# Kernel tuning notes

Measured on AMD Instinct MI355X. Metric: run time of the kernel, lower is better.

The kernel has to match this reference:

```python
import jax, jax.numpy as jnp
import numpy as np

N = 50000
E = 800000
D = 64  # d_s


def _mlp2(x, w1, b1, w2, b2):
    # Linear -> SiLU -> Linear
    return jax.nn.silu(x @ w1 + b1) @ w2 + b2


def setup_inputs() -> dict:
    key = jax.random.key(0)
    ks = jax.random.split(key, 20)
    s = jax.random.normal(ks[0], (N, D), jnp.float32)
    v = jax.random.normal(ks[1], (N, 3), jnp.float32)
    edge_index = jax.random.randint(ks[2], (2, E), 0, N, jnp.int32)
    edge_attr = jax.random.normal(ks[3], (E, D), jnp.float32)
    ev = jax.random.normal(ks[4], (E, 3), jnp.float32)
    edge_vec_unit = ev / jnp.linalg.norm(ev, axis=-1, keepdims=True)

    def lin(k, fan_in, fan_out):
        kw, kb = jax.random.split(k)
        lim = 1.0 / np.sqrt(fan_in)
        w = jax.random.uniform(kw, (fan_in, fan_out), jnp.float32, -lim, lim)
        b = jax.random.uniform(kb, (fan_out,), jnp.float32, -lim, lim)
        return w, b

    ng_w1, ng_b1 = lin(ks[5], D + 1, D)
    ng_w2, ng_b2 = lin(ks[6], D, D)
    eg_w1, eg_b1 = lin(ks[7], D + 1, D)
    eg_w2, eg_b2 = lin(ks[8], D, D)
    mg_w1, mg_b1 = lin(ks[9], 3 * D, 2 * D)
    mg_w2, mg_b2 = lin(ks[10], 2 * D, D)
    pe_w, pe_b = lin(ks[11], D, 1)
    up_w, up_b = lin(ks[12], D, D)
    ln_g = jnp.ones((D,), jnp.float32)
    ln_b = jnp.zeros((D,), jnp.float32)
    return dict(s=s, v=v, edge_index=edge_index, edge_attr=edge_attr,
                edge_vec_unit=edge_vec_unit,
                ng_w1=ng_w1, ng_b1=ng_b1, ng_w2=ng_w2, ng_b2=ng_b2,
                eg_w1=eg_w1, eg_b1=eg_b1, eg_w2=eg_w2, eg_b2=eg_b2,
                mg_w1=mg_w1, mg_b1=mg_b1, mg_w2=mg_w2, mg_b2=mg_b2,
                pe_w=pe_w, pe_b=pe_b, up_w=up_w, up_b=up_b,
                ln_g=ln_g, ln_b=ln_b)


def reference(s, v, edge_index, edge_attr, edge_vec_unit,
              ng_w1, ng_b1, ng_w2, ng_b2,
              eg_w1, eg_b1, eg_w2, eg_b2,
              mg_w1, mg_b1, mg_w2, mg_b2,
              pe_w, pe_b, up_w, up_b, ln_g, ln_b):
    row, col = edge_index[0], edge_index[1]
    s_i, s_j = s[row], s[col]            # (E, D)
    v_i, v_j = v[row], v[col]            # (E, 3)

    dot_ij = jnp.sum(v_i * edge_vec_unit, axis=-1, keepdims=True)
    dot_ji = jnp.sum(v_j * -edge_vec_unit, axis=-1, keepdims=True)
    res_ij = 1.0 - dot_ij
    res_ji = 1.0 - dot_ji
    cross_mag = jnp.linalg.norm(jnp.cross(v_i, v_j), axis=-1, keepdims=True)

    node_feat_i = _mlp2(jnp.concatenate([s_i, res_ij], -1), ng_w1, ng_b1, ng_w2, ng_b2)
    node_feat_j = _mlp2(jnp.concatenate([s_j, res_ji], -1), ng_w1, ng_b1, ng_w2, ng_b2)
    edge_feat = _mlp2(jnp.concatenate([edge_attr, cross_mag], -1), eg_w1, eg_b1, eg_w2, eg_b2)

    msg = _mlp2(jnp.concatenate([node_feat_i, node_feat_j, edge_feat], -1),
                mg_w1, mg_b1, mg_w2, mg_b2)   # (E, D)
    coeff = msg @ pe_w + pe_b                 # (E, 1)
    v_msg = edge_vec_unit * coeff             # (E, 3)

    n = s.shape[0]
    s_agg = jax.ops.segment_sum(msg, row, num_segments=n)    # (N, D)
    v_agg = jax.ops.segment_sum(v_msg, row, num_segments=n)  # (N, 3)

    s_new = s + jax.nn.silu(s_agg) @ up_w + up_b
    mu = jnp.mean(s_new, axis=-1, keepdims=True)
    var = jnp.var(s_new, axis=-1, keepdims=True)
    s_out = (s_new - mu) * jax.lax.rsqrt(var + 1e-5) * ln_g + ln_b

    v_new = v + v_agg
    denom = jnp.maximum(jnp.linalg.norm(v_new, axis=-1, keepdims=True), 1e-6)
    v_out = v_new / denom
    return (s_out, v_out)
```

## Files before the change

### kernel.cpp

```cpp
#include <hip/hip_runtime.h>
#include <math.h>

#define NN 50000
#define NE 800000
#define D 64

typedef __attribute__((ext_vector_type(8))) short short8;
typedef __attribute__((ext_vector_type(4))) float f32x4;

__device__ __forceinline__ float silu_f(float x) { return x / (1.0f + __expf(-x)); }

__device__ __forceinline__ unsigned int pack2(float a, float b) {
  unsigned int r;
  asm("v_cvt_pk_bf16_f32 %0, %1, %2" : "=v"(r) : "v"(a), "v"(b));
  return r;
}
__device__ __forceinline__ short8 pack_frag(f32x4 a, f32x4 b) {
  union { unsigned int u[4]; short8 s; } r;
  r.u[0] = pack2(a[0], a[1]);
  r.u[1] = pack2(a[2], a[3]);
  r.u[2] = pack2(b[0], b[1]);
  r.u[3] = pack2(b[2], b[3]);
  return r.s;
}

__global__ void prep_all(const float* __restrict__ ng_w2,
                         const float* __restrict__ eg_w1,
                         const float* __restrict__ eg_w2,
                         const float* __restrict__ mg_w1,
                         const float* __restrict__ mg_w2,
                         const float* __restrict__ ng_w1,
                         const float* __restrict__ up_w,
                         unsigned short* __restrict__ out) {
  int t = blockIdx.x * 256 + threadIdx.x;
  if (t >= 104 * 64) return;
  int frag = t >> 6, L = t & 63;
  const float* W; int K, N, f0;
  if (frag < 8)       { W = ng_w2; K = 64;  N = 64;  f0 = 0; }
  else if (frag < 16) { W = eg_w1; K = 64;  N = 64;  f0 = 8; }
  else if (frag < 24) { W = eg_w2; K = 64;  N = 64;  f0 = 16; }
  else if (frag < 72) { W = mg_w1; K = 192; N = 128; f0 = 24; }
  else if (frag < 88) { W = mg_w2; K = 128; N = 64;  f0 = 72; }
  else if (frag < 96) { W = ng_w1; K = 64;  N = 64;  f0 = 88; }
  else                { W = up_w;  K = 64;  N = 64;  f0 = 96; }
  int lf = frag - f0;
  int kd = K >> 5;
  int nt = lf / kd, ks = lf % kd;
  int kb = ks * 32 + (L >> 4) * 8;
  int nc = nt * 16 + (L & 15);
  unsigned int p[4];
#pragma unroll
  for (int jj = 0; jj < 4; ++jj) {
    float a = W[(size_t)(kb + 2 * jj) * N + nc];
    float b = W[(size_t)(kb + 2 * jj + 1) * N + nc];
    p[jj] = pack2(a, b);
  }
  *(uint4*)(out + (size_t)frag * 512 + L * 8) = make_uint4(p[0], p[1], p[2], p[3]);
}

__global__ __launch_bounds__(256, 4) void node_pre(
    const float* __restrict__ s, const float* __restrict__ ng_b1,
    const unsigned short* __restrict__ WF, float* __restrict__ h_ng,
    float* __restrict__ s_agg, float* __restrict__ v_agg) {
  __shared__ __align__(16) char sm[4 * 8704];
  int tid = threadIdx.x, w = tid >> 6, lane = tid & 63;
  int l15 = lane & 15, q = lane >> 4, fb = q * 8;
  char* my = sm + w * 8704;
  int nb = (blockIdx.x * 4 + w) * 32;
  if (nb >= NN) return;

  short8 Bs[2][2];
#pragma unroll
  for (int h = 0; h < 2; ++h)
#pragma unroll
    for (int kt = 0; kt < 2; ++kt) {
      int n = nb + h * 16 + l15; if (n >= NN) n = NN - 1;
      f32x4 x0 = *(const f32x4*)(s + (size_t)n * D + kt * 32 + fb);
      f32x4 x1 = *(const f32x4*)(s + (size_t)n * D + kt * 32 + fb + 4);
      Bs[h][kt] = pack_frag(x0, x1);
    }
  short8 F[4][2]; f32x4 bb[4];
#pragma unroll
  for (int mt = 0; mt < 4; ++mt) {
    F[mt][0] = *(const short8*)(WF + (size_t)(88 + mt * 2 + 0) * 512 + lane * 8);
    F[mt][1] = *(const short8*)(WF + (size_t)(88 + mt * 2 + 1) * 512 + lane * 8);
    bb[mt] = *(const f32x4*)(ng_b1 + mt * 16 + 4 * q);
  }
#pragma unroll
  for (int h = 0; h < 2; ++h)
#pragma unroll
    for (int mt = 0; mt < 4; ++mt) {
      f32x4 acc = {0.f, 0.f, 0.f, 0.f};
      acc = __builtin_amdgcn_mfma_f32_16x16x32_bf16(F[mt][0], Bs[h][0], acc, 0, 0, 0);
      acc = __builtin_amdgcn_mfma_f32_16x16x32_bf16(F[mt][1], Bs[h][1], acc, 0, 0, 0);
      acc[0] += bb[mt][0]; acc[1] += bb[mt][1]; acc[2] += bb[mt][2]; acc[3] += bb[mt][3];
      *(f32x4*)(my + (((h * 16 + l15) * 68 + mt * 16 + 4 * q) << 2)) = acc;
    }
#pragma unroll
  for (int h = 0; h < 2; ++h)
#pragma unroll
    for (int e = 0; e < 16; ++e) {
      int n = nb + h * 16 + e;
      if (n < NN) {
        float val = *(const float*)(my + (((h * 16 + e) * 68 + lane) << 2));
        h_ng[(size_t)n * D + lane] = val;
        s_agg[(size_t)n * D + lane] = 0.f;
      }
    }
#pragma unroll
  for (int h = 0; h < 2; ++h) {
    int n = nb + h * 16 + l15;
    if (q < 3 && n < NN) v_agg[(size_t)n * 3 + q] = 0.f;
  }
}

#define LSTR 100
#define LDSW (32 * LSTR * 4)

__global__ __launch_bounds__(256, 3) void edge_mfma(
    const float* __restrict__ v, const int* __restrict__ ei,
    const float* __restrict__ edge_attr, const float* __restrict__ evu,
    const float* __restrict__ ng_w1, const float* __restrict__ ng_b2,
    const float* __restrict__ eg_w1, const float* __restrict__ eg_b1,
    const float* __restrict__ eg_b2,
    const float* __restrict__ mg_b1, const float* __restrict__ mg_b2,
    const float* __restrict__ pe_w, const float* __restrict__ pe_b,
    const float* __restrict__ h_ng,
    const unsigned short* __restrict__ WF,
    float* __restrict__ s_agg, float* __restrict__ v_agg) {
  __shared__ __align__(16) char sm[4 * LDSW];
  int tid = threadIdx.x, w = tid >> 6, lane = tid & 63;
  int l15 = lane & 15, q = lane >> 4, fb = q * 8;
  char* my = sm + w * LDSW;
  int eb = (blockIdx.x * 4 + w) * 32;

  int rown[2], coln[2];
  float rij[2], rji[2], uu0[2], uu1[2], uu2[2], cmag[2];
#pragma unroll
  for (int h = 0; h < 2; ++h) {
    int e = eb + h * 16 + l15;
    int r = ei[e], c = ei[NE + e];
    rown[h] = r; coln[h] = c;
    float u0 = evu[e * 3 + 0], u1 = evu[e * 3 + 1], u2 = evu[e * 3 + 2];
    uu0[h] = u0; uu1[h] = u1; uu2[h] = u2;
    float vi0 = v[r * 3 + 0], vi1 = v[r * 3 + 1], vi2 = v[r * 3 + 2];
    float vj0 = v[c * 3 + 0], vj1 = v[c * 3 + 1], vj2 = v[c * 3 + 2];
    rij[h] = 1.f - (vi0 * u0 + vi1 * u1 + vi2 * u2);
    rji[h] = 1.f + (vj0 * u0 + vj1 * u1 + vj2 * u2);
    float cx = vi1 * vj2 - vi2 * vj1;
    float cy = vi2 * vj0 - vi0 * vj2;
    float cz = vi0 * vj1 - vi1 * vj0;
    cmag[h] = sqrtf(cx * cx + cy * cy + cz * cz);
  }

  short8 Bai[2][2], Baj[2][2], Bxe[2][2];
  f32x4 w1l[2][2];
#pragma unroll
  for (int kt = 0; kt < 2; ++kt) {
    w1l[kt][0] = *(const f32x4*)(ng_w1 + 64 * 64 + kt * 32 + fb);
    w1l[kt][1] = *(const f32x4*)(ng_w1 + 64 * 64 + kt * 32 + fb + 4);
  }
#pragma unroll
  for (int h = 0; h < 2; ++h)
#pragma unroll
    for (int kt = 0; kt < 2; ++kt) {
      const float* pr = h_ng + (size_t)rown[h] * D + kt * 32 + fb;
      const float* pc = h_ng + (size_t)coln[h] * D + kt * 32 + fb;
      const float* px = edge_attr + (size_t)(eb + h * 16 + l15) * D + kt * 32 + fb;
      f32x4 a0 = *(const f32x4*)pr, a1 = *(const f32x4*)(pr + 4);
      f32x4 b0 = *(const f32x4*)pc, b1 = *(const f32x4*)(pc + 4);
      f32x4 x0 = *(const f32x4*)px, x1 = *(const f32x4*)(px + 4);
      f32x4 si0, si1, sj0, sj1;
#pragma unroll
      for (int c2 = 0; c2 < 4; ++c2) {
        si0[c2] = silu_f(a0[c2] + rij[h] * w1l[kt][0][c2]);
        si1[c2] = silu_f(a1[c2] + rij[h] * w1l[kt][1][c2]);
        sj0[c2] = silu_f(b0[c2] + rji[h] * w1l[kt][0][c2]);
        sj1[c2] = silu_f(b1[c2] + rji[h] * w1l[kt][1][c2]);
      }
      Bai[h][kt] = pack_frag(si0, si1);
      Baj[h][kt] = pack_frag(sj0, sj1);
      Bxe[h][kt] = pack_frag(x0, x1);
    }

  {
    short8 F[4][2]; f32x4 bb[4];
#pragma unroll
    for (int mt = 0; mt < 4; ++mt) {
      F[mt][0] = *(const short8*)(WF + (size_t)(0 + mt * 2 + 0) * 512 + lane * 8);
      F[mt][1] = *(const short8*)(WF + (size_t)(0 + mt * 2 + 1) * 512 + lane * 8);
      bb[mt] = *(const f32x4*)(ng_b2 + mt * 16 + 4 * q);
    }
#pragma unroll
    for (int h = 0; h < 2; ++h)
#pragma unroll
      for (int mt = 0; mt < 4; ++mt) {
        f32x4 ai = {0.f, 0.f, 0.f, 0.f}, aj = {0.f, 0.f, 0.f, 0.f};
        ai = __builtin_amdgcn_mfma_f32_16x16x32_bf16(F[mt][0], Bai[h][0], ai, 0, 0, 0);
        ai = __builtin_amdgcn_mfma_f32_16x16x32_bf16(F[mt][1], Bai[h][1], ai, 0, 0, 0);
        aj = __builtin_amdgcn_mfma_f32_16x16x32_bf16(F[mt][0], Baj[h][0], aj, 0, 0, 0);
        aj = __builtin_amdgcn_mfma_f32_16x16x32_bf16(F[mt][1], Baj[h][1], aj, 0, 0, 0);
        uint2 pi, pj;
        pi.x = pack2(ai[0] + bb[mt][0], ai[1] + bb[mt][1]);
        pi.y = pack2(ai[2] + bb[mt][2], ai[3] + bb[mt][3]);
        pj.x = pack2(aj[0] + bb[mt][0], aj[1] + bb[mt][1]);
        pj.y = pack2(aj[2] + bb[mt][2], aj[3] + bb[mt][3]);
        int row = h * 16 + l15;
        *(uint2*)(my + ((row * LSTR + mt * 8 + 2 * q) << 2)) = pi;
        *(uint2*)(my + ((row * LSTR + 32 + mt * 8 + 2 * q) << 2)) = pj;
      }
  }

  {
    short8 F[4][2]; f32x4 bb[4], el[4];
#pragma unroll
    for (int mt = 0; mt < 4; ++mt) {
      F[mt][0] = *(const short8*)(WF + (size_t)(8 + mt * 2 + 0) * 512 + lane * 8);
      F[mt][1] = *(const short8*)(WF + (size_t)(8 + mt * 2 + 1) * 512 + lane * 8);
      bb[mt] = *(const f32x4*)(eg_b1 + mt * 16 + 4 * q);
      el[mt] = *(const f32x4*)(eg_w1 + 64 * 64 + mt * 16 + 4 * q);
    }
#pragma unroll
    for (int h = 0; h < 2; ++h)
#pragma unroll
      for (int mt = 0; mt < 4; ++mt) {
        f32x4 acc = {0.f, 0.f, 0.f, 0.f};
        acc = __builtin_amdgcn_mfma_f32_16x16x32_bf16(F[mt][0], Bxe[h][0], acc, 0, 0, 0);
        acc = __builtin_amdgcn_mfma_f32_16x16x32_bf16(F[mt][1], Bxe[h][1], acc, 0, 0, 0);
        float t0 = silu_f(acc[0] + bb[mt][0] + cmag[h] * el[mt][0]);
        float t1 = silu_f(acc[1] + bb[mt][1] + cmag[h] * el[mt][1]);
        float t2 = silu_f(acc[2] + bb[mt][2] + cmag[h] * el[mt][2]);
        float t3 = silu_f(acc[3] + bb[mt][3] + cmag[h] * el[mt][3]);
        uint2 p; p.x = pack2(t0, t1); p.y = pack2(t2, t3);
        *(uint2*)(my + (((h * 16 + l15) * LSTR + 64 + mt * 8 + 2 * q) << 2)) = p;
      }
  }

  {
    short8 Bae[2][2];
#pragma unroll
    for (int h = 0; h < 2; ++h)
#pragma unroll
      for (int kt = 0; kt < 2; ++kt)
        Bae[h][kt] = *(const short8*)(my + (((h * 16 + l15) * LSTR + 64 + 16 * kt + 4 * q) << 2));
    short8 F[4][2]; f32x4 bb[4];
#pragma unroll
    for (int mt = 0; mt < 4; ++mt) {
      F[mt][0] = *(const short8*)(WF + (size_t)(16 + mt * 2 + 0) * 512 + lane * 8);
      F[mt][1] = *(const short8*)(WF + (size_t)(16 + mt * 2 + 1) * 512 + lane * 8);
      bb[mt] = *(const f32x4*)(eg_b2 + mt * 16 + 4 * q);
    }
#pragma unroll
    for (int h = 0; h < 2; ++h)
#pragma unroll
      for (int mt = 0; mt < 4; ++mt) {
        f32x4 acc = {0.f, 0.f, 0.f, 0.f};
        acc = __builtin_amdgcn_mfma_f32_16x16x32_bf16(F[mt][0], Bae[h][0], acc, 0, 0, 0);
        acc = __builtin_amdgcn_mfma_f32_16x16x32_bf16(F[mt][1], Bae[h][1], acc, 0, 0, 0);
        uint2 p;
        p.x = pack2(acc[0] + bb[mt][0], acc[1] + bb[mt][1]);
        p.y = pack2(acc[2] + bb[mt][2], acc[3] + bb[mt][3]);
        *(uint2*)(my + (((h * 16 + l15) * LSTR + 64 + mt * 8 + 2 * q) << 2)) = p;
      }
  }

  {
    short8 Bin[2][6];
#pragma unroll
    for (int h = 0; h < 2; ++h)
#pragma unroll
      for (int kt = 0; kt < 6; ++kt)
        Bin[h][kt] = *(const short8*)(my + (((h * 16 + l15) * LSTR + 16 * kt + 4 * q) << 2));
#pragma unroll
    for (int mt = 0; mt < 8; ++mt) {
      short8 F[6];
#pragma unroll
      for (int ks = 0; ks < 6; ++ks)
        F[ks] = *(const short8*)(WF + (size_t)(24 + mt * 6 + ks) * 512 + lane * 8);
      f32x4 bb = *(const f32x4*)(mg_b1 + mt * 16 + 4 * q);
#pragma unroll
      for (int h = 0; h < 2; ++h) {
        f32x4 acc = {0.f, 0.f, 0.f, 0.f};
#pragma unroll
        for (int ks = 0; ks < 6; ++ks)
          acc = __builtin_amdgcn_mfma_f32_16x16x32_bf16(F[ks], Bin[h][ks], acc, 0, 0, 0);
        uint2 p;
        p.x = pack2(silu_f(acc[0] + bb[0]), silu_f(acc[1] + bb[1]));
        p.y = pack2(silu_f(acc[2] + bb[2]), silu_f(acc[3] + bb[3]));
        *(uint2*)(my + (((h * 16 + l15) * LSTR + mt * 8 + 2 * q) << 2)) = p;
      }
    }
  }

  f32x4 msg[2][4];
  {
    short8 Bh[2][4];
#pragma unroll
    for (int h = 0; h < 2; ++h)
#pragma unroll
      for (int kt = 0; kt < 4; ++kt)
        Bh[h][kt] = *(const short8*)(my + (((h * 16 + l15) * LSTR + 16 * kt + 4 * q) << 2));
#pragma unroll
    for (int mt = 0; mt < 4; ++mt) {
      short8 F[4];
#pragma unroll
      for (int ks = 0; ks < 4; ++ks)
        F[ks] = *(const short8*)(WF + (size_t)(72 + mt * 4 + ks) * 512 + lane * 8);
      f32x4 bb = *(const f32x4*)(mg_b2 + mt * 16 + 4 * q);
#pragma unroll
      for (int h = 0; h < 2; ++h) {
        f32x4 acc = {0.f, 0.f, 0.f, 0.f};
#pragma unroll
        for (int ks = 0; ks < 4; ++ks)
          acc = __builtin_amdgcn_mfma_f32_16x16x32_bf16(F[ks], Bh[h][ks], acc, 0, 0, 0);
        acc[0] += bb[0]; acc[1] += bb[1]; acc[2] += bb[2]; acc[3] += bb[3];
        msg[h][mt] = acc;
      }
    }
  }

  float part[2] = {0.f, 0.f};
#pragma unroll
  for (int mt = 0; mt < 4; ++mt) {
    f32x4 pw4 = *(const f32x4*)(pe_w + mt * 16 + 4 * q);
#pragma unroll
    for (int h = 0; h < 2; ++h)
      part[h] += msg[h][mt][0] * pw4[0] + msg[h][mt][1] * pw4[1] +
                 msg[h][mt][2] * pw4[2] + msg[h][mt][3] * pw4[3];
  }
  float peb = pe_b[0];
#pragma unroll
  for (int h = 0; h < 2; ++h) {
    part[h] += __shfl_xor(part[h], 16, 64);
    part[h] += __shfl_xor(part[h], 32, 64);
    if (q < 3) {
      float uc = (q == 0) ? uu0[h] : ((q == 1) ? uu1[h] : uu2[h]);
      atomicAdd(&v_agg[(size_t)rown[h] * 3 + q], uc * (part[h] + peb));
    }
  }

#pragma unroll
  for (int h = 0; h < 2; ++h)
#pragma unroll
    for (int mt = 0; mt < 4; ++mt)
      *(f32x4*)(my + (((h * 16 + l15) * LSTR + mt * 16 + 4 * q) << 2)) = msg[h][mt];
#pragma unroll
  for (int h = 0; h < 2; ++h)
#pragma unroll
    for (int e = 0; e < 16; ++e) {
      int sr = __builtin_amdgcn_readlane(rown[h], e);
      float val = *(const float*)(my + (((h * 16 + e) * LSTR + lane) << 2));
      atomicAdd(&s_agg[(size_t)sr * D + lane], val);
    }
}

__global__ __launch_bounds__(256, 4) void node_out(
    const float* __restrict__ s, const float* __restrict__ v,
    const float* __restrict__ up_b,
    const float* __restrict__ ln_g, const float* __restrict__ ln_b,
    const float* __restrict__ s_agg, const float* __restrict__ v_agg,
    const unsigned short* __restrict__ WF, float* __restrict__ out) {
  __shared__ __align__(16) char sm[4 * 8704];
  int tid = threadIdx.x, w = tid >> 6, lane = tid & 63;
  int l15 = lane & 15, q = lane >> 4, fb = q * 8;
  char* my = sm + w * 8704;
  int nb = (blockIdx.x * 4 + w) * 32;
  if (nb >= NN) return;

  short8 Bg[2][2];
#pragma unroll
  for (int h = 0; h < 2; ++h)
#pragma unroll
    for (int kt = 0; kt < 2; ++kt) {
      int n = nb + h * 16 + l15; if (n >= NN) n = NN - 1;
      f32x4 g0 = *(const f32x4*)(s_agg + (size_t)n * D + kt * 32 + fb);
      f32x4 g1 = *(const f32x4*)(s_agg + (size_t)n * D + kt * 32 + fb + 4);
#pragma unroll
      for (int c2 = 0; c2 < 4; ++c2) { g0[c2] = silu_f(g0[c2]); g1[c2] = silu_f(g1[c2]); }
      Bg[h][kt] = pack_frag(g0, g1);
    }
  short8 F[4][2]; f32x4 bb[4];
#pragma unroll
  for (int mt = 0; mt < 4; ++mt) {
    F[mt][0] = *(const short8*)(WF + (size_t)(96 + mt * 2 + 0) * 512 + lane * 8);
    F[mt][1] = *(const short8*)(WF + (size_t)(96 + mt * 2 + 1) * 512 + lane * 8);
    bb[mt] = *(const f32x4*)(up_b + mt * 16 + 4 * q);
  }
  f32x4 sn[2][4];
#pragma unroll
  for (int h = 0; h < 2; ++h) {
    int n = nb + h * 16 + l15; if (n >= NN) n = NN - 1;
#pragma unroll
    for (int mt = 0; mt < 4; ++mt) {
      f32x4 acc = {0.f, 0.f, 0.f, 0.f};
      acc = __builtin_amdgcn_mfma_f32_16x16x32_bf16(F[mt][0], Bg[h][0], acc, 0, 0, 0);
      acc = __builtin_amdgcn_mfma_f32_16x16x32_bf16(F[mt][1], Bg[h][1], acc, 0, 0, 0);
      f32x4 sv = *(const f32x4*)(s + (size_t)n * D + mt * 16 + 4 * q);
      sn[h][mt][0] = acc[0] + bb[mt][0] + sv[0];
      sn[h][mt][1] = acc[1] + bb[mt][1] + sv[1];
      sn[h][mt][2] = acc[2] + bb[mt][2] + sv[2];
      sn[h][mt][3] = acc[3] + bb[mt][3] + sv[3];
    }
  }
#pragma unroll
  for (int h = 0; h < 2; ++h) {
    float m = 0.f;
#pragma unroll
    for (int mt = 0; mt < 4; ++mt)
      m += sn[h][mt][0] + sn[h][mt][1] + sn[h][mt][2] + sn[h][mt][3];
    m += __shfl_xor(m, 16, 64);
    m += __shfl_xor(m, 32, 64);
    float mu = m * (1.f / 64.f);
    float vv = 0.f;
#pragma unroll
    for (int mt = 0; mt < 4; ++mt)
#pragma unroll
      for (int r = 0; r < 4; ++r) {
        float d = sn[h][mt][r] - mu;
        vv += d * d;
      }
    vv += __shfl_xor(vv, 16, 64);
    vv += __shfl_xor(vv, 32, 64);
    float inv = 1.f / sqrtf(vv * (1.f / 64.f) + 1e-5f);
#pragma unroll
    for (int mt = 0; mt < 4; ++mt) {
      f32x4 lg = *(const f32x4*)(ln_g + mt * 16 + 4 * q);
      f32x4 lb = *(const f32x4*)(ln_b + mt * 16 + 4 * q);
      f32x4 ov;
#pragma unroll
      for (int r = 0; r < 4; ++r) ov[r] = (sn[h][mt][r] - mu) * inv * lg[r] + lb[r];
      *(f32x4*)(my + (((h * 16 + l15) * 68 + mt * 16 + 4 * q) << 2)) = ov;
    }
  }
#pragma unroll
  for (int h = 0; h < 2; ++h)
#pragma unroll
    for (int e = 0; e < 16; ++e) {
      int n = nb + h * 16 + e;
      if (n < NN) {
        float val = *(const float*)(my + (((h * 16 + e) * 68 + lane) << 2));
        out[(size_t)n * D + lane] = val;
      }
    }
#pragma unroll
  for (int h = 0; h < 2; ++h) {
    int n = nb + h * 16 + l15;
    if (q < 3 && n < NN) {
      float v0 = v[n * 3 + 0] + v_agg[(size_t)n * 3 + 0];
      float v1 = v[n * 3 + 1] + v_agg[(size_t)n * 3 + 1];
      float v2 = v[n * 3 + 2] + v_agg[(size_t)n * 3 + 2];
      float nrm = sqrtf(v0 * v0 + v1 * v1 + v2 * v2);
      float denom = fmaxf(nrm, 1e-6f);
      float val = (q == 0) ? v0 : ((q == 1) ? v1 : v2);
      out[(size_t)NN * D + (size_t)n * 3 + q] = val / denom;
    }
  }
}

extern "C" void kernel_launch(void* const* d_in, const int* in_sizes, int n_in,
                              void* d_out, int out_size, void* d_ws, size_t ws_size,
                              hipStream_t stream) {
  const float* s         = (const float*)d_in[0];
  const float* v         = (const float*)d_in[1];
  const int*   ei        = (const int*)d_in[2];
  const float* edge_attr = (const float*)d_in[3];
  const float* evu       = (const float*)d_in[4];
  const float* ng_w1     = (const float*)d_in[5];
  const float* ng_b1     = (const float*)d_in[6];
  const float* ng_w2     = (const float*)d_in[7];
  const float* ng_b2     = (const float*)d_in[8];
  const float* eg_w1     = (const float*)d_in[9];
  const float* eg_b1     = (const float*)d_in[10];
  const float* eg_w2     = (const float*)d_in[11];
  const float* eg_b2     = (const float*)d_in[12];
  const float* mg_w1     = (const float*)d_in[13];
  const float* mg_b1     = (const float*)d_in[14];
  const float* mg_w2     = (const float*)d_in[15];
  const float* mg_b2     = (const float*)d_in[16];
  const float* pe_w      = (const float*)d_in[17];
  const float* pe_b      = (const float*)d_in[18];
  const float* up_w      = (const float*)d_in[19];
  const float* up_b      = (const float*)d_in[20];
  const float* ln_g      = (const float*)d_in[21];
  const float* ln_b      = (const float*)d_in[22];
  (void)in_sizes; (void)n_in; (void)out_size; (void)ws_size;

  float* out   = (float*)d_out;
  float* s_agg = (float*)d_ws;
  float* v_agg = s_agg + (size_t)NN * D;
  unsigned short* WF = (unsigned short*)(v_agg + (size_t)NN * 3);
  float* h_ng  = out;

  prep_all<<<26, 256, 0, stream>>>(ng_w2, eg_w1, eg_w2, mg_w1, mg_w2, ng_w1, up_w, WF);

  int node_blocks = (NN + 127) / 128;
  node_pre<<<node_blocks, 256, 0, stream>>>(s, ng_b1, WF, h_ng, s_agg, v_agg);

  edge_mfma<<<NE / 128, 256, 0, stream>>>(
      v, ei, edge_attr, evu,
      ng_w1, ng_b2, eg_w1, eg_b1, eg_b2,
      mg_b1, mg_b2, pe_w, pe_b, h_ng, WF, s_agg, v_agg);

  node_out<<<node_blocks, 256, 0, stream>>>(
      s, v, up_b, ln_g, ln_b, s_agg, v_agg, WF, out);
}
```

Measured before the change: 573.9 us.

## Replace s_agg float atomics with CSR bucketed messages and segmented reduction

Builds a per-row histogram and prefix scan, then has the edge kernel write each message into a row-bucketed slot claimed via an atomic cursor instead of doing 64 float atomicAdds per edge into s_agg. A separate wave-per-node kernel sums each row's contiguous messages. This aims to remove heavy atomic contention, at the cost of writing and rereading a 205 MB message buffer plus extra histogram and single-block scan launches. The CSR path is used only when the workspace is large enough, otherwise the old atomic path runs.

```diff
diff --git a/kernel.cpp b/kernel.cpp
--- a/kernel.cpp
+++ b/kernel.cpp
@@ -58,10 +58,49 @@
   *(uint4*)(out + (size_t)frag * 512 + L * 8) = make_uint4(p[0], p[1], p[2], p[3]);
 }
 
+__global__ void hist_k(const int* __restrict__ ei, int* __restrict__ cnt) {
+  int e = blockIdx.x * 256 + threadIdx.x;
+  if (e < NE) atomicAdd(&cnt[ei[e]], 1);
+}
+
+#define SCAN_CH ((NN + 255) / 256)
+__global__ __launch_bounds__(256) void scan_k(const int* __restrict__ cnt,
+                                              int* __restrict__ row_start,
+                                              int* __restrict__ cursor) {
+  __shared__ int wsum[4];
+  int t = threadIdx.x;
+  int lane = t & 63, w = t >> 6;
+  int base = t * SCAN_CH;
+  int s = 0;
+  for (int i = 0; i < SCAN_CH; ++i) {
+    int b = base + i;
+    if (b < NN) s += cnt[b];
+  }
+  int v = s;
+#pragma unroll
+  for (int off = 1; off < 64; off <<= 1) {
+    int y = __shfl_up(v, off, 64);
+    if (lane >= off) v += y;
+  }
+  if (lane == 63) wsum[w] = v;
+  __syncthreads();
+  int woff = 0;
+  for (int i = 0; i < w; ++i) woff += wsum[i];
+  int run = woff + v - s;
+  for (int i = 0; i < SCAN_CH; ++i) {
+    int b = base + i;
+    if (b < NN) {
+      row_start[b] = run;
+      cursor[b] = run;
+      run += cnt[b];
+    }
+  }
+  if (t == 255) row_start[NN] = run;
+}
+
 __global__ __launch_bounds__(256, 4) void node_pre(
     const float* __restrict__ s, const float* __restrict__ ng_b1,
-    const unsigned short* __restrict__ WF, float* __restrict__ h_ng,
-    float* __restrict__ s_agg, float* __restrict__ v_agg) {
+    const unsigned short* __restrict__ WF, float* __restrict__ h_ng) {
   __shared__ __align__(16) char sm[4 * 8704];
   int tid = threadIdx.x, w = tid >> 6, lane = tid & 63;
   int l15 = lane & 15, q = lane >> 4, fb = q * 8;
@@ -104,19 +143,14 @@
       if (n < NN) {
         float val = *(const float*)(my + (((h * 16 + e) * 68 + lane) << 2));
         h_ng[(size_t)n * D + lane] = val;
-        s_agg[(size_t)n * D + lane] = 0.f;
-      }
-    }
-#pragma unroll
-  for (int h = 0; h < 2; ++h) {
-    int n = nb + h * 16 + l15;
-    if (q < 3 && n < NN) v_agg[(size_t)n * 3 + q] = 0.f;
-  }
+      }
+    }
 }
 
 #define LSTR 100
 #define LDSW (32 * LSTR * 4)
 
+template <bool CSR>
 __global__ __launch_bounds__(256, 3) void edge_mfma(
     const float* __restrict__ v, const int* __restrict__ ei,
     const float* __restrict__ edge_attr, const float* __restrict__ evu,
@@ -127,7 +161,8 @@
     const float* __restrict__ pe_w, const float* __restrict__ pe_b,
     const float* __restrict__ h_ng,
     const unsigned short* __restrict__ WF,
-    float* __restrict__ s_agg, float* __restrict__ v_agg) {
+    float* __restrict__ s_agg, float* __restrict__ v_agg,
+    float* __restrict__ msg_sorted, int* __restrict__ cursor) {
   __shared__ __align__(16) char sm[4 * LDSW];
   int tid = threadIdx.x, w = tid >> 6, lane = tid & 63;
   int l15 = lane & 15, q = lane >> 4, fb = q * 8;
@@ -339,19 +374,55 @@
     }
   }
 
+  int slotv[2];
+  if (CSR) {
+#pragma unroll
+    for (int h = 0; h < 2; ++h)
+      if (q == 0) slotv[h] = atomicAdd(&cursor[rown[h]], 1);
+  }
+
 #pragma unroll
   for (int h = 0; h < 2; ++h)
 #pragma unroll
     for (int mt = 0; mt < 4; ++mt)
       *(f32x4*)(my + (((h * 16 + l15) * LSTR + mt * 16 + 4 * q) << 2)) = msg[h][mt];
-#pragma unroll
-  for (int h = 0; h < 2; ++h)
-#pragma unroll
-    for (int e = 0; e < 16; ++e) {
-      int sr = __builtin_amdgcn_readlane(rown[h], e);
-      float val = *(const float*)(my + (((h * 16 + e) * LSTR + lane) << 2));
-      atomicAdd(&s_agg[(size_t)sr * D + lane], val);
-    }
+
+  if (CSR) {
+#pragma unroll
+    for (int h = 0; h < 2; ++h)
+#pragma unroll
+      for (int e = 0; e < 16; ++e) {
+        int slot = __builtin_amdgcn_readlane(slotv[h], e);
+        float val = *(const float*)(my + (((h * 16 + e) * LSTR + lane) << 2));
+        msg_sorted[(size_t)slot * D + lane] = val;
+      }
+  } else {
+#pragma unroll
+    for (int h = 0; h < 2; ++h)
+#pragma unroll
+      for (int e = 0; e < 16; ++e) {
+        int sr = __builtin_amdgcn_readlane(rown[h], e);
+        float val = *(const float*)(my + (((h * 16 + e) * LSTR + lane) << 2));
+        atomicAdd(&s_agg[(size_t)sr * D + lane], val);
+      }
+  }
+}
+
+__global__ __launch_bounds__(256) void aggregate_k(
+    const float* __restrict__ msg_sorted, const int* __restrict__ row_start,
+    float* __restrict__ s_agg) {
+  int wid = (blockIdx.x * 256 + threadIdx.x) >> 6;
+  int lane = threadIdx.x & 63;
+  if (wid >= NN) return;
+  int s0 = row_start[wid], s1 = row_start[wid + 1];
+  float acc = 0.f, acc2 = 0.f;
+  int r = s0;
+  for (; r + 1 < s1; r += 2) {
+    acc  += msg_sorted[(size_t)r * D + lane];
+    acc2 += msg_sorted[(size_t)(r + 1) * D + lane];
+  }
+  if (r < s1) acc += msg_sorted[(size_t)r * D + lane];
+  s_agg[(size_t)wid * D + lane] = acc + acc2;
 }
 
 __global__ __launch_bounds__(256, 4) void node_out(
@@ -483,23 +554,56 @@
   const float* up_b      = (const float*)d_in[20];
   const float* ln_g      = (const float*)d_in[21];
   const float* ln_b      = (const float*)d_in[22];
-  (void)in_sizes; (void)n_in; (void)out_size; (void)ws_size;
-
-  float* out   = (float*)d_out;
-  float* s_agg = (float*)d_ws;
-  float* v_agg = s_agg + (size_t)NN * D;
-  unsigned short* WF = (unsigned short*)(v_agg + (size_t)NN * 3);
-  float* h_ng  = out;
+  (void)in_sizes; (void)n_in; (void)out_size;
+
+  float* out = (float*)d_out;
+  char* ws = (char*)d_ws;
+  size_t o = 0;
+  auto carve = [&](size_t bytes) {
+    char* p = ws + o;
+    o = (o + bytes + 255) & ~(size_t)255;
+    return p;
+  };
+  float* s_agg          = (float*)carve((size_t)NN * D * 4);
+  float* v_agg          = (float*)carve((size_t)NN * 3 * 4);
+  unsigned short* WF    = (unsigned short*)carve((size_t)104 * 512 * 2);
+  int* cnt              = (int*)carve((size_t)NN * 4);
+  int* cursor           = (int*)carve((size_t)NN * 4);
+  int* row_start        = (int*)carve((size_t)(NN + 1) * 4);
+  float* msg_sorted     = (float*)carve((size_t)NE * D * 4);
+  bool use_csr = (ws_size >= o);
+
+  float* h_ng = out;
+
+  hipMemsetAsync(v_agg, 0, (size_t)NN * 3 * 4, stream);
+  if (use_csr) {
+    hipMemsetAsync(cnt, 0, (size_t)NN * 4, stream);
+  } else {
+    hipMemsetAsync(s_agg, 0, (size_t)NN * D * 4, stream);
+  }
 
   prep_all<<<26, 256, 0, stream>>>(ng_w2, eg_w1, eg_w2, mg_w1, mg_w2, ng_w1, up_w, WF);
 
+  if (use_csr) {
+    hist_k<<<(NE + 255) / 256, 256, 0, stream>>>(ei, cnt);
+    scan_k<<<1, 256, 0, stream>>>(cnt, row_start, cursor);
+  }
+
   int node_blocks = (NN + 127) / 128;
-  node_pre<<<node_blocks, 256, 0, stream>>>(s, ng_b1, WF, h_ng, s_agg, v_agg);
-
-  edge_mfma<<<NE / 128, 256, 0, stream>>>(
-      v, ei, edge_attr, evu,
-      ng_w1, ng_b2, eg_w1, eg_b1, eg_b2,
-      mg_b1, mg_b2, pe_w, pe_b, h_ng, WF, s_agg, v_agg);
+  node_pre<<<node_blocks, 256, 0, stream>>>(s, ng_b1, WF, h_ng);
+
+  if (use_csr) {
+    edge_mfma<true><<<NE / 128, 256, 0, stream>>>(
+        v, ei, edge_attr, evu,
+        ng_w1, ng_b2, eg_w1, eg_b1, eg_b2,
+        mg_b1, mg_b2, pe_w, pe_b, h_ng, WF, s_agg, v_agg, msg_sorted, cursor);
+    aggregate_k<<<(NN * 64 + 255) / 256, 256, 0, stream>>>(msg_sorted, row_start, s_agg);
+  } else {
+    edge_mfma<false><<<NE / 128, 256, 0, stream>>>(
+        v, ei, edge_attr, evu,
+        ng_w1, ng_b2, eg_w1, eg_b1, eg_b2,
+        mg_b1, mg_b2, pe_w, pe_b, h_ng, WF, s_agg, v_agg, msg_sorted, cursor);
+  }
 
   node_out<<<node_blocks, 256, 0, stream>>>(
       s, v, up_b, ln_g, ln_b, s_agg, v_agg, WF, out);
```

Measured after the change: 784.8 us. +36.7%, slower.

## Fold second-layer linear weights into message MLP first layer

Applied to the files above, without the earlier changes.

The second linear layers of the node and edge gates (ng_w2, eg_w2) are pre-multiplied into the matching blocks of mg_w1 on device, and their biases are folded into one combined bias. The edge kernel then feeds the post-SiLU hidden activations straight into the message MLP's first layer with a K=192 contraction, which removes three GEMM stages and their LDS round-trips. The smaller LDS staging buffer raises occupancy from 3 to 4 blocks per SM. The trade-off is extra rounding, since the combined weights are computed in fp32 and then cast to bf16 rather than rounding each stage separately.

```diff
diff --git a/kernel.cpp b/kernel.cpp
--- a/kernel.cpp
+++ b/kernel.cpp
@@ -24,28 +24,50 @@
   return r.s;
 }
 
-__global__ void prep_all(const float* __restrict__ ng_w2,
-                         const float* __restrict__ eg_w1,
-                         const float* __restrict__ eg_w2,
-                         const float* __restrict__ mg_w1,
+__global__ void prep_comb(const float* __restrict__ ng_w2,
+                          const float* __restrict__ eg_w2,
+                          const float* __restrict__ mg_w1,
+                          const float* __restrict__ mg_b1,
+                          const float* __restrict__ ng_b2,
+                          const float* __restrict__ eg_b2,
+                          float* __restrict__ W_comb, float* __restrict__ bprime) {
+  int t = blockIdx.x * 256 + threadIdx.x;
+  if (t < 3 * 64 * 128) {
+    int src = t / (64 * 128);
+    int r = t % (64 * 128);
+    int k = r >> 7, m = r & 127;
+    const float* A = (src == 2) ? eg_w2 : ng_w2;
+    const float* M = mg_w1 + (size_t)(src * 64) * 128 + m;
+    float acc = 0.f;
+    for (int n = 0; n < 64; ++n) acc += A[k * 64 + n] * M[(size_t)n * 128];
+    W_comb[t] = acc;
+  }
+  if (t < 128) {
+    float acc = mg_b1[t];
+    for (int n = 0; n < 64; ++n)
+      acc += ng_b2[n] * (mg_w1[(size_t)n * 128 + t] + mg_w1[(size_t)(64 + n) * 128 + t]) +
+             eg_b2[n] * mg_w1[(size_t)(128 + n) * 128 + t];
+    bprime[t] = acc;
+  }
+}
+
+__global__ void prep_all(const float* __restrict__ eg_w1,
                          const float* __restrict__ mg_w2,
                          const float* __restrict__ ng_w1,
                          const float* __restrict__ up_w,
+                         const float* __restrict__ W_comb,
                          unsigned short* __restrict__ out) {
   int t = blockIdx.x * 256 + threadIdx.x;
-  if (t >= 104 * 64) return;
+  if (t >= 88 * 64) return;
   int frag = t >> 6, L = t & 63;
-  const float* W; int K, N, f0;
-  if (frag < 8)       { W = ng_w2; K = 64;  N = 64;  f0 = 0; }
-  else if (frag < 16) { W = eg_w1; K = 64;  N = 64;  f0 = 8; }
-  else if (frag < 24) { W = eg_w2; K = 64;  N = 64;  f0 = 16; }
-  else if (frag < 72) { W = mg_w1; K = 192; N = 128; f0 = 24; }
-  else if (frag < 88) { W = mg_w2; K = 128; N = 64;  f0 = 72; }
-  else if (frag < 96) { W = ng_w1; K = 64;  N = 64;  f0 = 88; }
-  else                { W = up_w;  K = 64;  N = 64;  f0 = 96; }
-  int lf = frag - f0;
-  int kd = K >> 5;
-  int nt = lf / kd, ks = lf % kd;
+  const float* W; int N, nt, ks;
+  if (frag < 8)       { int lf = frag;      W = eg_w1; N = 64;  nt = lf >> 1; ks = lf & 1; }
+  else if (frag < 56) { int lf = frag - 8;  int mt = lf / 6, s2 = lf % 6;
+                        W = W_comb + (size_t)(s2 >> 1) * (64 * 128); N = 128;
+                        nt = mt; ks = s2 & 1; }
+  else if (frag < 72) { int lf = frag - 56; W = mg_w2; N = 64;  nt = lf >> 2; ks = lf & 3; }
+  else if (frag < 80) { int lf = frag - 72; W = ng_w1; N = 64;  nt = lf >> 1; ks = lf & 1; }
+  else                { int lf = frag - 80; W = up_w;  N = 64;  nt = lf >> 1; ks = lf & 1; }
   int kb = ks * 32 + (L >> 4) * 8;
   int nc = nt * 16 + (L & 15);
   unsigned int p[4];
@@ -82,8 +104,8 @@
   short8 F[4][2]; f32x4 bb[4];
 #pragma unroll
   for (int mt = 0; mt < 4; ++mt) {
-    F[mt][0] = *(const short8*)(WF + (size_t)(88 + mt * 2 + 0) * 512 + lane * 8);
-    F[mt][1] = *(const short8*)(WF + (size_t)(88 + mt * 2 + 1) * 512 + lane * 8);
+    F[mt][0] = *(const short8*)(WF + (size_t)(72 + mt * 2 + 0) * 512 + lane * 8);
+    F[mt][1] = *(const short8*)(WF + (size_t)(72 + mt * 2 + 1) * 512 + lane * 8);
     bb[mt] = *(const f32x4*)(ng_b1 + mt * 16 + 4 * q);
   }
 #pragma unroll
@@ -114,16 +136,15 @@
   }
 }
 
-#define LSTR 100
+#define LSTR 68
 #define LDSW (32 * LSTR * 4)
 
-__global__ __launch_bounds__(256, 3) void edge_mfma(
+__global__ __launch_bounds__(256, 4) void edge_mfma(
     const float* __restrict__ v, const int* __restrict__ ei,
     const float* __restrict__ edge_attr, const float* __restrict__ evu,
-    const float* __restrict__ ng_w1, const float* __restrict__ ng_b2,
-    const float* __restrict__ eg_w1, const float* __restrict__ eg_b1,
-    const float* __restrict__ eg_b2,
-    const float* __restrict__ mg_b1, const float* __restrict__ mg_b2,
+    const float* __restrict__ ng_w1, const float* __restrict__ eg_w1,
+    const float* __restrict__ eg_b1, const float* __restrict__ bprime,
+    const float* __restrict__ mg_b2,
     const float* __restrict__ pe_w, const float* __restrict__ pe_b,
     const float* __restrict__ h_ng,
     const unsigned short* __restrict__ WF,
@@ -184,39 +205,11 @@
     }
 
   {
-    short8 F[4][2]; f32x4 bb[4];
+    short8 F[4][2]; f32x4 bb[4], el[4];
 #pragma unroll
     for (int mt = 0; mt < 4; ++mt) {
       F[mt][0] = *(const short8*)(WF + (size_t)(0 + mt * 2 + 0) * 512 + lane * 8);
       F[mt][1] = *(const short8*)(WF + (size_t)(0 + mt * 2 + 1) * 512 + lane * 8);
-      bb[mt] = *(const f32x4*)(ng_b2 + mt * 16 + 4 * q);
-    }
-#pragma unroll
-    for (int h = 0; h < 2; ++h)
-#pragma unroll
-      for (int mt = 0; mt < 4; ++mt) {
-        f32x4 ai = {0.f, 0.f, 0.f, 0.f}, aj = {0.f, 0.f, 0.f, 0.f};
-        ai = __builtin_amdgcn_mfma_f32_16x16x32_bf16(F[mt][0], Bai[h][0], ai, 0, 0, 0);
-        ai = __builtin_amdgcn_mfma_f32_16x16x32_bf16(F[mt][1], Bai[h][1], ai, 0, 0, 0);
-        aj = __builtin_amdgcn_mfma_f32_16x16x32_bf16(F[mt][0], Baj[h][0], aj, 0, 0, 0);
-        aj = __builtin_amdgcn_mfma_f32_16x16x32_bf16(F[mt][1], Baj[h][1], aj, 0, 0, 0);
-        uint2 pi, pj;
-        pi.x = pack2(ai[0] + bb[mt][0], ai[1] + bb[mt][1]);
-        pi.y = pack2(ai[2] + bb[mt][2], ai[3] + bb[mt][3]);
-        pj.x = pack2(aj[0] + bb[mt][0], aj[1] + bb[mt][1]);
-        pj.y = pack2(aj[2] + bb[mt][2], aj[3] + bb[mt][3]);
-        int row = h * 16 + l15;
-        *(uint2*)(my + ((row * LSTR + mt * 8 + 2 * q) << 2)) = pi;
-        *(uint2*)(my + ((row * LSTR + 32 + mt * 8 + 2 * q) << 2)) = pj;
-      }
-  }
-
-  {
-    short8 F[4][2]; f32x4 bb[4], el[4];
-#pragma unroll
-    for (int mt = 0; mt < 4; ++mt) {
-      F[mt][0] = *(const short8*)(WF + (size_t)(8 + mt * 2 + 0) * 512 + lane * 8);
-      F[mt][1] = *(const short8*)(WF + (size_t)(8 + mt * 2 + 1) * 512 + lane * 8);
       bb[mt] = *(const f32x4*)(eg_b1 + mt * 16 + 4 * q);
       el[mt] = *(const f32x4*)(eg_w1 + 64 * 64 + mt * 16 + 4 * q);
     }
@@ -232,63 +225,37 @@
         float t2 = silu_f(acc[2] + bb[mt][2] + cmag[h] * el[mt][2]);
         float t3 = silu_f(acc[3] + bb[mt][3] + cmag[h] * el[mt][3]);
         uint2 p; p.x = pack2(t0, t1); p.y = pack2(t2, t3);
-        *(uint2*)(my + (((h * 16 + l15) * LSTR + 64 + mt * 8 + 2 * q) << 2)) = p;
-      }
-  }
-
-  {
-    short8 Bae[2][2];
-#pragma unroll
-    for (int h = 0; h < 2; ++h)
-#pragma unroll
-      for (int kt = 0; kt < 2; ++kt)
-        Bae[h][kt] = *(const short8*)(my + (((h * 16 + l15) * LSTR + 64 + 16 * kt + 4 * q) << 2));
-    short8 F[4][2]; f32x4 bb[4];
-#pragma unroll
-    for (int mt = 0; mt < 4; ++mt) {
-      F[mt][0] = *(const short8*)(WF + (size_t)(16 + mt * 2 + 0) * 512 + lane * 8);
-      F[mt][1] = *(const short8*)(WF + (size_t)(16 + mt * 2 + 1) * 512 + lane * 8);
-      bb[mt] = *(const f32x4*)(eg_b2 + mt * 16 + 4 * q);
-    }
-#pragma unroll
-    for (int h = 0; h < 2; ++h)
-#pragma unroll
-      for (int mt = 0; mt < 4; ++mt) {
-        f32x4 acc = {0.f, 0.f, 0.f, 0.f};
-        acc = __builtin_amdgcn_mfma_f32_16x16x32_bf16(F[mt][0], Bae[h][0], acc, 0, 0, 0);
-        acc = __builtin_amdgcn_mfma_f32_16x16x32_bf16(F[mt][1], Bae[h][1], acc, 0, 0, 0);
-        uint2 p;
-        p.x = pack2(acc[0] + bb[mt][0], acc[1] + bb[mt][1]);
-        p.y = pack2(acc[2] + bb[mt][2], acc[3] + bb[mt][3]);
-        *(uint2*)(my + (((h * 16 + l15) * LSTR + 64 + mt * 8 + 2 * q) << 2)) = p;
-      }
-  }
-
-  {
-    short8 Bin[2][6];
-#pragma unroll
-    for (int h = 0; h < 2; ++h)
-#pragma unroll
-      for (int kt = 0; kt < 6; ++kt)
-        Bin[h][kt] = *(const short8*)(my + (((h * 16 + l15) * LSTR + 16 * kt + 4 * q) << 2));
-#pragma unroll
-    for (int mt = 0; mt < 8; ++mt) {
-      short8 F[6];
-#pragma unroll
-      for (int ks = 0; ks < 6; ++ks)
-        F[ks] = *(const short8*)(WF + (size_t)(24 + mt * 6 + ks) * 512 + lane * 8);
-      f32x4 bb = *(const f32x4*)(mg_b1 + mt * 16 + 4 * q);
-#pragma unroll
-      for (int h = 0; h < 2; ++h) {
-        f32x4 acc = {0.f, 0.f, 0.f, 0.f};
-#pragma unroll
-        for (int ks = 0; ks < 6; ++ks)
-          acc = __builtin_amdgcn_mfma_f32_16x16x32_bf16(F[ks], Bin[h][ks], acc, 0, 0, 0);
-        uint2 p;
-        p.x = pack2(silu_f(acc[0] + bb[0]), silu_f(acc[1] + bb[1]));
-        p.y = pack2(silu_f(acc[2] + bb[2]), silu_f(acc[3] + bb[3]));
         *(uint2*)(my + (((h * 16 + l15) * LSTR + mt * 8 + 2 * q) << 2)) = p;
       }
+  }
+
+  short8 Bae[2][2];
+#pragma unroll
+  for (int h = 0; h < 2; ++h)
+#pragma unroll
+    for (int kt = 0; kt < 2; ++kt)
+      Bae[h][kt] = *(const short8*)(my + (((h * 16 + l15) * LSTR + 16 * kt + 4 * q) << 2));
+
+#pragma unroll
+  for (int mt = 0; mt < 8; ++mt) {
+    short8 F[6];
+#pragma unroll
+    for (int s2 = 0; s2 < 6; ++s2)
+      F[s2] = *(const short8*)(WF + (size_t)(8 + mt * 6 + s2) * 512 + lane * 8);
+    f32x4 bb = *(const f32x4*)(bprime + mt * 16 + 4 * q);
+#pragma unroll
+    for (int h = 0; h < 2; ++h) {
+      f32x4 acc = {0.f, 0.f, 0.f, 0.f};
+      acc = __builtin_amdgcn_mfma_f32_16x16x32_bf16(F[0], Bai[h][0], acc, 0, 0, 0);
+      acc = __builtin_amdgcn_mfma_f32_16x16x32_bf16(F[1], Bai[h][1], acc, 0, 0, 0);
+      acc = __builtin_amdgcn_mfma_f32_16x16x32_bf16(F[2], Baj[h][0], acc, 0, 0, 0);
+      acc = __builtin_amdgcn_mfma_f32_16x16x32_bf16(F[3], Baj[h][1], acc, 0, 0, 0);
+      acc = __builtin_amdgcn_mfma_f32_16x16x32_bf16(F[4], Bae[h][0], acc, 0, 0, 0);
+      acc = __builtin_amdgcn_mfma_f32_16x16x32_bf16(F[5], Bae[h][1], acc, 0, 0, 0);
+      uint2 p;
+      p.x = pack2(silu_f(acc[0] + bb[0]), silu_f(acc[1] + bb[1]));
+      p.y = pack2(silu_f(acc[2] + bb[2]), silu_f(acc[3] + bb[3]));
+      *(uint2*)(my + (((h * 16 + l15) * LSTR + mt * 8 + 2 * q) << 2)) = p;
     }
   }
 
@@ -305,7 +272,7 @@
       short8 F[4];
 #pragma unroll
       for (int ks = 0; ks < 4; ++ks)
-        F[ks] = *(const short8*)(WF + (size_t)(72 + mt * 4 + ks) * 512 + lane * 8);
+        F[ks] = *(const short8*)(WF + (size_t)(56 + mt * 4 + ks) * 512 + lane * 8);
       f32x4 bb = *(const f32x4*)(mg_b2 + mt * 16 + 4 * q);
 #pragma unroll
       for (int h = 0; h < 2; ++h) {
@@ -382,8 +349,8 @@
   short8 F[4][2]; f32x4 bb[4];
 #pragma unroll
   for (int mt = 0; mt < 4; ++mt) {
-    F[mt][0] = *(const short8*)(WF + (size_t)(96 + mt * 2 + 0) * 512 + lane * 8);
-    F[mt][1] = *(const short8*)(WF + (size_t)(96 + mt * 2 + 1) * 512 + lane * 8);
+    F[mt][0] = *(const short8*)(WF + (size_t)(80 + mt * 2 + 0) * 512 + lane * 8);
+    F[mt][1] = *(const short8*)(WF + (size_t)(80 + mt * 2 + 1) * 512 + lane * 8);
     bb[mt] = *(const f32x4*)(up_b + mt * 16 + 4 * q);
   }
   f32x4 sn[2][4];
@@ -485,21 +452,33 @@
   const float* ln_b      = (const float*)d_in[22];
   (void)in_sizes; (void)n_in; (void)out_size; (void)ws_size;
 
-  float* out   = (float*)d_out;
-  float* s_agg = (float*)d_ws;
-  float* v_agg = s_agg + (size_t)NN * D;
-  unsigned short* WF = (unsigned short*)(v_agg + (size_t)NN * 3);
-  float* h_ng  = out;
-
-  prep_all<<<26, 256, 0, stream>>>(ng_w2, eg_w1, eg_w2, mg_w1, mg_w2, ng_w1, up_w, WF);
+  float* out = (float*)d_out;
+  char* ws = (char*)d_ws;
+  size_t o = 0;
+  auto carve = [&](size_t bytes) {
+    char* p = ws + o;
+    o = (o + bytes + 255) & ~(size_t)255;
+    return p;
+  };
+  float* s_agg       = (float*)carve((size_t)NN * D * 4);
+  float* v_agg       = (float*)carve((size_t)NN * 3 * 4);
+  unsigned short* WF = (unsigned short*)carve((size_t)88 * 512 * 2);
+  float* W_comb      = (float*)carve((size_t)3 * 64 * 128 * 4);
+  float* bprime      = (float*)carve((size_t)128 * 4);
+
+  float* h_ng = out;
+
+  prep_comb<<<96, 256, 0, stream>>>(ng_w2, eg_w2, mg_w1, mg_b1, ng_b2, eg_b2,
+                                    W_comb, bprime);
+  prep_all<<<22, 256, 0, stream>>>(eg_w1, mg_w2, ng_w1, up_w, W_comb, WF);
 
   int node_blocks = (NN + 127) / 128;
   node_pre<<<node_blocks, 256, 0, stream>>>(s, ng_b1, WF, h_ng, s_agg, v_agg);
 
   edge_mfma<<<NE / 128, 256, 0, stream>>>(
       v, ei, edge_attr, evu,
-      ng_w1, ng_b2, eg_w1, eg_b1, eg_b2,
-      mg_b1, mg_b2, pe_w, pe_b, h_ng, WF, s_agg, v_agg);
+      ng_w1, eg_w1, eg_b1, bprime, mg_b2,
+      pe_w, pe_b, h_ng, WF, s_agg, v_agg);
 
   node_out<<<node_blocks, 256, 0, stream>>>(
       s, v, up_b, ln_g, ln_b, s_agg, v_agg, WF, out);
```

Result: slower. 619.4 us (+7.9%).
